# Kernel optimization log

Hardware: AMD Instinct MI355X
Metric: run time of the kernel (lower is better)

The kernel has to match this reference:

```python
import jax, jax.numpy as jnp
import numpy as np

IGNORE_INDEX = -100
BT, H, V = 2048, 4096, 32000


def setup_inputs() -> dict:
    key = jax.random.key(0)
    k1, k2, k3, k4 = jax.random.split(key, 4)
    _input = jax.random.normal(k1, (BT, H), dtype=jnp.float32) * 0.02
    lin_weight = jax.random.normal(k2, (V, H), dtype=jnp.float32) * 0.02
    bias = jnp.zeros((V,), dtype=jnp.float32)
    target = jax.random.randint(k3, (BT,), 0, V)
    loss_weights = jax.random.uniform(k4, (BT,), dtype=jnp.float32)
    reduce_sum_loss_weights = jnp.sum(loss_weights)  # scalar float32
    return {
        "lin_weight": lin_weight,
        "_input": _input,
        "target": target,
        "bias": bias,
        "loss_weights": loss_weights,
        "reduce_sum_loss_weights": reduce_sum_loss_weights,
        "grad_accumulation_steps": 1,
    }


def reference(lin_weight, _input, target, bias, loss_weights,
              reduce_sum_loss_weights, grad_accumulation_steps):
    # logits: (BT, V) -- the torch module chunks over BT to avoid materializing
    # this; as a correctness reference we compute it directly.
    logits = _input @ lin_weight.T + bias
    mask = target != IGNORE_INDEX                      # (BT,)
    n_non_ignore = jnp.maximum(mask.sum(), 1).astype(logits.dtype)
    safe_t = jnp.where(mask, target, 0)
    lse = jax.nn.logsumexp(logits, axis=-1)            # (BT,)
    gold = jnp.take_along_axis(logits, safe_t[:, None], axis=-1)[:, 0]
    # liger kernel with reduction='mean' divides per-row loss by n_non_ignore
    loss_1d = jnp.where(mask, (lse - gold) / n_non_ignore, 0.0)
    total = jnp.sum(loss_1d * loss_weights)
    rs = jnp.asarray(reduce_sum_loss_weights).reshape(())
    denom = jnp.where(rs == 0, 1.0, rs)
    loss = jnp.where(rs == 0, 0.0, total / denom)
    return loss / grad_accumulation_steps
```

## Files before the change

### kernel.cpp

```cpp
#include <hip/hip_runtime.h>
#include <hip/hip_bf16.h>
#include <math.h>

#define IGNORE_INDEX (-100)

constexpr int BT = 2048, H = 4096, V = 32000;
constexpr int BM = 256, BN = 256, BK = 64;
constexpr int KT = H / BK;
constexpr int MT2 = BT / BM;
constexpr int NT2 = V / BN;
constexpr int NCHUNK = NT2 * 4;

typedef int   i32x4  __attribute__((ext_vector_type(4)));
typedef int   i32x8  __attribute__((ext_vector_type(8)));
typedef float f32x16 __attribute__((ext_vector_type(16)));

#define SC8 120

__device__ __forceinline__ void gload_lds16(const char* g, char* l) {
  __builtin_amdgcn_global_load_lds(
      (const __attribute__((address_space(1))) unsigned int*)(g),
      (__attribute__((address_space(3))) unsigned int*)(l), 16, 0, 0);
}

#define BAR()        asm volatile("s_barrier" ::: "memory")
#define WAIT_VM(N)   asm volatile("s_waitcnt vmcnt(" #N ")" ::: "memory")
#define SB0()        __builtin_amdgcn_sched_barrier(0)

__global__ __launch_bounds__(256)
void convert_fp8(const float* __restrict__ src, char* __restrict__ dst,
                 int n8) {
  int i = blockIdx.x * blockDim.x + threadIdx.x;
  const int stride = gridDim.x * blockDim.x;
  for (; i < n8; i += stride) {
    const float4 f0 = ((const float4*)src)[2 * i];
    const float4 f1 = ((const float4*)src)[2 * i + 1];
    const float S = 128.f;
    int lo = 0, hi = 0;
    lo = __builtin_amdgcn_cvt_pk_fp8_f32(f0.x * S, f0.y * S, lo, false);
    lo = __builtin_amdgcn_cvt_pk_fp8_f32(f0.z * S, f0.w * S, lo, true);
    hi = __builtin_amdgcn_cvt_pk_fp8_f32(f1.x * S, f1.y * S, hi, false);
    hi = __builtin_amdgcn_cvt_pk_fp8_f32(f1.z * S, f1.w * S, hi, true);
    int2 v; v.x = lo; v.y = hi;
    ((int2*)dst)[i] = v;
  }
}

__global__ __launch_bounds__(512, 2)
void gemm_lse_3buf(const char* __restrict__ Wq,
                   const char* __restrict__ Xq,
                   const int* __restrict__ target,
                   const float* __restrict__ bias,
                   float* __restrict__ pM, float* __restrict__ pS,
                   float* __restrict__ gold)
{
  __shared__ char As[49152];
  __shared__ char Bs[49152];

  const int tid  = threadIdx.x;
  const int lane = tid & 63;
  const int wid  = tid >> 6;
  const int wr   = wid >> 2;
  const int wcol = wid & 3;

  const int bid = (int)blockIdx.x;
  const int swz = (bid & 7) * 125 + (bid >> 3);
  const int mt = swz & (MT2 - 1);
  const int nt = swz >> 3;
  const int m0 = mt * BM, n0 = nt * BN;

  const int l31 = lane & 31;
  const int h   = lane >> 5;
  const int r2  = (l31 >> 1) & 3;
  const int s0  = ((2 * h) ^ r2) << 4;
  const int s1  = ((2 * h + 1) ^ r2) << 4;
  const int abase = (wr * 128 + l31) * 64;
  const int bbase = (wcol * 64 + l31) * 64;

  const int srow  = lane >> 2;
  const int sslot = ((lane & 3) ^ ((lane >> 3) & 3)) << 4;

  const char* asrc = Xq + (size_t)(m0 + wid * 32 + srow) * H + sslot;
  const char* bsrc = Wq + (size_t)(n0 + wid * 32 + srow) * H + sslot;

  f32x16 acc[4][2] = {};
  i32x8 aF0, aF1, bF0, bF1;

#define STAGE_A(BUF, DT)                                                      \
  { gload_lds16(asrc + (DT) * BK,                                             \
                &As[(BUF) * 16384 + wid * 2048 + lane * 16]);                 \
    gload_lds16(asrc + (size_t)16 * H + (DT) * BK,                            \
                &As[(BUF) * 16384 + wid * 2048 + 1024 + lane * 16]); }

#define STAGE_B(BUF, DT)                                                      \
  { gload_lds16(bsrc + (DT) * BK,                                             \
                &Bs[(BUF) * 16384 + wid * 2048 + lane * 16]);                 \
    gload_lds16(bsrc + (size_t)16 * H + (DT) * BK,                            \
                &Bs[(BUF) * 16384 + wid * 2048 + 1024 + lane * 16]); }

#define RDA(DST, BUF, MI)                                                     \
  { i32x4 lo = *(const i32x4*)&As[(BUF) * 16384 + abase + (MI) * 2048 + s0];  \
    i32x4 hi = *(const i32x4*)&As[(BUF) * 16384 + abase + (MI) * 2048 + s1];  \
    DST[0] = lo[0]; DST[1] = lo[1]; DST[2] = lo[2]; DST[3] = lo[3];           \
    DST[4] = hi[0]; DST[5] = hi[1]; DST[6] = hi[2]; DST[7] = hi[3]; }

#define RDB(DST, BUF, NJ)                                                     \
  { i32x4 lo = *(const i32x4*)&Bs[(BUF) * 16384 + bbase + (NJ) * 2048 + s0];  \
    i32x4 hi = *(const i32x4*)&Bs[(BUF) * 16384 + bbase + (NJ) * 2048 + s1];  \
    DST[0] = lo[0]; DST[1] = lo[1]; DST[2] = lo[2]; DST[3] = lo[3];           \
    DST[4] = hi[0]; DST[5] = hi[1]; DST[6] = hi[2]; DST[7] = hi[3]; }

#define MFMA4(MH)                                                             \
  { __builtin_amdgcn_s_setprio(1);                                            \
    acc[(MH)*2+0][0] = __builtin_amdgcn_mfma_scale_f32_32x32x64_f8f6f4(       \
        aF0, bF0, acc[(MH)*2+0][0], 0, 0, 0, SC8, 0, SC8);                    \
    acc[(MH)*2+0][1] = __builtin_amdgcn_mfma_scale_f32_32x32x64_f8f6f4(       \
        aF0, bF1, acc[(MH)*2+0][1], 0, 0, 0, SC8, 0, SC8);                    \
    acc[(MH)*2+1][0] = __builtin_amdgcn_mfma_scale_f32_32x32x64_f8f6f4(       \
        aF1, bF0, acc[(MH)*2+1][0], 0, 0, 0, SC8, 0, SC8);                    \
    acc[(MH)*2+1][1] = __builtin_amdgcn_mfma_scale_f32_32x32x64_f8f6f4(       \
        aF1, bF1, acc[(MH)*2+1][1], 0, 0, 0, SC8, 0, SC8);                    \
    __builtin_amdgcn_s_setprio(0); }

#define PHASE(D, DOSTAGE, VMN)                                                \
  { if (DOSTAGE) { STAGE_B(((D) + 2) % 3, (D) + 2);                           \
                   STAGE_A(((D) + 2) % 3, (D) + 2); }                         \
    WAIT_VM(VMN);                                                             \
    RDA(aF0, (D) % 3, 0); RDA(aF1, (D) % 3, 1);                               \
    RDB(bF0, (D) % 3, 0); RDB(bF1, (D) % 3, 1);                               \
    MFMA4(0);                                                                 \
    RDA(aF0, (D) % 3, 2); RDA(aF1, (D) % 3, 3);                               \
    MFMA4(1);                                                                 \
    SB0(); BAR(); }

  STAGE_B(0, 0); STAGE_A(0, 0);
  STAGE_B(1, 1); STAGE_A(1, 1);
  WAIT_VM(4);
  BAR();

  for (int it = 0; it < 20; ++it) {
    PHASE(0, 1, 4);
    PHASE(1, 1, 4);
    PHASE(2, 1, 4);
    asrc += 3 * BK; bsrc += 3 * BK;
  }
  PHASE(0, 1, 4);
  PHASE(1, 1, 0);
  PHASE(2, 0, 0);
  RDA(aF0, 0, 0); RDA(aF1, 0, 1); RDB(bF0, 0, 0); RDB(bF1, 0, 1);
  MFMA4(0);
  RDA(aF0, 0, 2); RDA(aF1, 0, 3);
  MFMA4(1);

#undef PHASE
#undef STAGE_A
#undef STAGE_B
#undef RDA
#undef RDB
#undef MFMA4

  const int colbase = n0 + wcol * 64;
  float bv[2];
#pragma unroll
  for (int nj = 0; nj < 2; ++nj) bv[nj] = bias[colbase + nj * 32 + l31];

  const int chunk = nt * 4 + wcol;
#pragma unroll
  for (int mi = 0; mi < 4; ++mi) {
#pragma unroll
    for (int r = 0; r < 16; ++r) {
      const int row = m0 + wr * 128 + mi * 32 + (r & 3) + 8 * (r >> 2) + 4 * h;
      const float v0 = acc[mi][0][r] + bv[0];
      const float v1 = acc[mi][1][r] + bv[1];
      float mx = fmaxf(v0, v1);
#pragma unroll
      for (int d = 1; d < 32; d <<= 1) mx = fmaxf(mx, __shfl_xor(mx, d));
      float s = expf(v0 - mx) + expf(v1 - mx);
#pragma unroll
      for (int d = 1; d < 32; d <<= 1) s += __shfl_xor(s, d);
      if (l31 == 0) {
        pM[(size_t)row * NCHUNK + chunk] = mx;
        pS[(size_t)row * NCHUNK + chunk] = s;
      }
      const int t = target[row];
      const int d0 = t - colbase;
      if (d0 >= 0 && d0 < 64 && l31 == (d0 & 31)) {
        gold[row] = (d0 >> 5) ? v1 : v0;
      }
    }
  }
}

__global__ __launch_bounds__(256)
void reduce_lse(const float* __restrict__ pM, const float* __restrict__ pS,
                const float* __restrict__ gold, const int* __restrict__ target,
                const float* __restrict__ lw, float* __restrict__ rowterm)
{
  const int wid = threadIdx.x >> 6, lane = threadIdx.x & 63;
  const int row = blockIdx.x * 4 + wid;
  if (row >= BT) return;
  const float* pm = pM + (size_t)row * NCHUNK;
  const float* ps = pS + (size_t)row * NCHUNK;
  float m = -INFINITY;
  for (int c2 = lane; c2 < NCHUNK; c2 += 64) m = fmaxf(m, pm[c2]);
#pragma unroll
  for (int d = 1; d < 64; d <<= 1) m = fmaxf(m, __shfl_xor(m, d));
  float s = 0.f;
  for (int c2 = lane; c2 < NCHUNK; c2 += 64) s += ps[c2] * expf(pm[c2] - m);
#pragma unroll
  for (int d = 1; d < 64; d <<= 1) s += __shfl_xor(s, d);
  if (lane == 0) {
    const int t = target[row];
    float term = 0.f;
    if (t != IGNORE_INDEX) term = (m + logf(s) - gold[row]) * lw[row];
    rowterm[row] = term;
  }
}

__global__ __launch_bounds__(256)
void finalize(const float* __restrict__ rowterm, const int* __restrict__ target,
              const float* __restrict__ rsw, const int* __restrict__ gas,
              float* __restrict__ out)
{
  __shared__ float sred[4];
  __shared__ int cred[4];
  const int tid = threadIdx.x;
  float s = 0.f;
  int cnt = 0;
  for (int i = tid; i < BT; i += 256) {
    s += rowterm[i];
    cnt += (target[i] != IGNORE_INDEX) ? 1 : 0;
  }
#pragma unroll
  for (int d = 1; d < 64; d <<= 1) {
    s += __shfl_xor(s, d);
    cnt += __shfl_xor(cnt, d);
  }
  const int wid = tid >> 6, lane = tid & 63;
  if (lane == 0) { sred[wid] = s; cred[wid] = cnt; }
  __syncthreads();
  if (tid == 0) {
    const float st = sred[0] + sred[1] + sred[2] + sred[3];
    const int ct = cred[0] + cred[1] + cred[2] + cred[3];
    const float n = (float)((ct > 0) ? ct : 1);
    const float rs = rsw[0];
    float loss = (rs == 0.f) ? 0.f : (st / n) / rs;
    loss /= (float)gas[0];
    out[0] = loss;
  }
}

extern "C" void kernel_launch(void* const* d_in, const int* in_sizes, int n_in,
                              void* d_out, int out_size, void* d_ws, size_t ws_size,
                              hipStream_t stream)
{
  const float* Wt     = (const float*)d_in[0];
  const float* X      = (const float*)d_in[1];
  const int*   target = (const int*)d_in[2];
  const float* bias   = (const float*)d_in[3];
  const float* lw     = (const float*)d_in[4];
  const float* rsw    = (const float*)d_in[5];
  const int*   gas    = (const int*)d_in[6];
  float* out = (float*)d_out;

  const size_t nW = (size_t)V * H, nX = (size_t)BT * H;

  char* Wq = (char*)d_ws;
  char* Xq = Wq + nW;
  float* pM = (float*)(Xq + nX);
  float* pS = pM + (size_t)BT * NCHUNK;
  float* gold = pS + (size_t)BT * NCHUNK;
  float* rowterm = gold + BT;

  convert_fp8<<<dim3(2048), dim3(256), 0, stream>>>(Wt, Wq, (int)(nW / 8));
  convert_fp8<<<dim3(256), dim3(256), 0, stream>>>(X, Xq, (int)(nX / 8));
  gemm_lse_3buf<<<dim3(MT2 * NT2), dim3(512), 0, stream>>>(Wq, Xq, target,
                                                           bias, pM, pS, gold);
  reduce_lse<<<dim3(BT / 4), dim3(256), 0, stream>>>(pM, pS, gold, target, lw,
                                                     rowterm);
  finalize<<<dim3(1), dim3(256), 0, stream>>>(rowterm, target, rsw, gas, out);
}
```

Measured before the change: 600.5 us.

## Shrink GEMM tiles to 128x128 with 4 waves and move barrier before reads

Replaces the 256x256, 8-wave block tile with a 128x128, 4-wave tile and three blocks per CU, quadrupling the grid and halving accumulator state per wave. The barrier now sits after the load wait and before the LDS reads instead of at the end of each phase. The aim is better occupancy and tail balance across CUs. In exchange each block reuses less data from LDS, so global and L2 traffic rises, and with only one barrier per phase there is a possible race on buffer reuse.

```diff
diff --git a/kernel.cpp b/kernel.cpp
--- a/kernel.cpp
+++ b/kernel.cpp
@@ -5,11 +5,11 @@
 #define IGNORE_INDEX (-100)
 
 constexpr int BT = 2048, H = 4096, V = 32000;
-constexpr int BM = 256, BN = 256, BK = 64;
+constexpr int BM = 128, BN = 128, BK = 64;
 constexpr int KT = H / BK;
-constexpr int MT2 = BT / BM;
-constexpr int NT2 = V / BN;
-constexpr int NCHUNK = NT2 * 4;
+constexpr int MT = BT / BM;
+constexpr int NT = V / BN;
+constexpr int NCHUNK = NT * 2;
 
 typedef int   i32x4  __attribute__((ext_vector_type(4)));
 typedef int   i32x8  __attribute__((ext_vector_type(8)));
@@ -46,27 +46,27 @@
   }
 }
 
-__global__ __launch_bounds__(512, 2)
-void gemm_lse_3buf(const char* __restrict__ Wq,
-                   const char* __restrict__ Xq,
-                   const int* __restrict__ target,
-                   const float* __restrict__ bias,
-                   float* __restrict__ pM, float* __restrict__ pS,
-                   float* __restrict__ gold)
-{
-  __shared__ char As[49152];
-  __shared__ char Bs[49152];
+__global__ __launch_bounds__(256, 3)
+void gemm_lse_o3(const char* __restrict__ Wq,
+                 const char* __restrict__ Xq,
+                 const int* __restrict__ target,
+                 const float* __restrict__ bias,
+                 float* __restrict__ pM, float* __restrict__ pS,
+                 float* __restrict__ gold)
+{
+  __shared__ char As[24576];
+  __shared__ char Bs[24576];
 
   const int tid  = threadIdx.x;
   const int lane = tid & 63;
   const int wid  = tid >> 6;
-  const int wr   = wid >> 2;
-  const int wcol = wid & 3;
+  const int wr   = wid >> 1;
+  const int wc   = wid & 1;
 
   const int bid = (int)blockIdx.x;
-  const int swz = (bid & 7) * 125 + (bid >> 3);
-  const int mt = swz & (MT2 - 1);
-  const int nt = swz >> 3;
+  const int swz = (bid & 7) * 500 + (bid >> 3);
+  const int mt = swz & (MT - 1);
+  const int nt = swz >> 4;
   const int m0 = mt * BM, n0 = nt * BN;
 
   const int l31 = lane & 31;
@@ -74,8 +74,8 @@
   const int r2  = (l31 >> 1) & 3;
   const int s0  = ((2 * h) ^ r2) << 4;
   const int s1  = ((2 * h + 1) ^ r2) << 4;
-  const int abase = (wr * 128 + l31) * 64;
-  const int bbase = (wcol * 64 + l31) * 64;
+  const int abase = (wr * 64 + l31) * 64;
+  const int bbase = (wc * 64 + l31) * 64;
 
   const int srow  = lane >> 2;
   const int sslot = ((lane & 3) ^ ((lane >> 3) & 3)) << 4;
@@ -83,60 +83,57 @@
   const char* asrc = Xq + (size_t)(m0 + wid * 32 + srow) * H + sslot;
   const char* bsrc = Wq + (size_t)(n0 + wid * 32 + srow) * H + sslot;
 
-  f32x16 acc[4][2] = {};
+  f32x16 acc[2][2] = {};
   i32x8 aF0, aF1, bF0, bF1;
 
 #define STAGE_A(BUF, DT)                                                      \
   { gload_lds16(asrc + (DT) * BK,                                             \
-                &As[(BUF) * 16384 + wid * 2048 + lane * 16]);                 \
+                &As[(BUF) * 8192 + wid * 2048 + lane * 16]);                  \
     gload_lds16(asrc + (size_t)16 * H + (DT) * BK,                            \
-                &As[(BUF) * 16384 + wid * 2048 + 1024 + lane * 16]); }
+                &As[(BUF) * 8192 + wid * 2048 + 1024 + lane * 16]); }
 
 #define STAGE_B(BUF, DT)                                                      \
   { gload_lds16(bsrc + (DT) * BK,                                             \
-                &Bs[(BUF) * 16384 + wid * 2048 + lane * 16]);                 \
+                &Bs[(BUF) * 8192 + wid * 2048 + lane * 16]);                  \
     gload_lds16(bsrc + (size_t)16 * H + (DT) * BK,                            \
-                &Bs[(BUF) * 16384 + wid * 2048 + 1024 + lane * 16]); }
+                &Bs[(BUF) * 8192 + wid * 2048 + 1024 + lane * 16]); }
 
 #define RDA(DST, BUF, MI)                                                     \
-  { i32x4 lo = *(const i32x4*)&As[(BUF) * 16384 + abase + (MI) * 2048 + s0];  \
-    i32x4 hi = *(const i32x4*)&As[(BUF) * 16384 + abase + (MI) * 2048 + s1];  \
+  { i32x4 lo = *(const i32x4*)&As[(BUF) * 8192 + abase + (MI) * 2048 + s0];   \
+    i32x4 hi = *(const i32x4*)&As[(BUF) * 8192 + abase + (MI) * 2048 + s1];   \
     DST[0] = lo[0]; DST[1] = lo[1]; DST[2] = lo[2]; DST[3] = lo[3];           \
     DST[4] = hi[0]; DST[5] = hi[1]; DST[6] = hi[2]; DST[7] = hi[3]; }
 
 #define RDB(DST, BUF, NJ)                                                     \
-  { i32x4 lo = *(const i32x4*)&Bs[(BUF) * 16384 + bbase + (NJ) * 2048 + s0];  \
-    i32x4 hi = *(const i32x4*)&Bs[(BUF) * 16384 + bbase + (NJ) * 2048 + s1];  \
+  { i32x4 lo = *(const i32x4*)&Bs[(BUF) * 8192 + bbase + (NJ) * 2048 + s0];   \
+    i32x4 hi = *(const i32x4*)&Bs[(BUF) * 8192 + bbase + (NJ) * 2048 + s1];   \
     DST[0] = lo[0]; DST[1] = lo[1]; DST[2] = lo[2]; DST[3] = lo[3];           \
     DST[4] = hi[0]; DST[5] = hi[1]; DST[6] = hi[2]; DST[7] = hi[3]; }
 
-#define MFMA4(MH)                                                             \
+#define MFMA4()                                                               \
   { __builtin_amdgcn_s_setprio(1);                                            \
-    acc[(MH)*2+0][0] = __builtin_amdgcn_mfma_scale_f32_32x32x64_f8f6f4(       \
-        aF0, bF0, acc[(MH)*2+0][0], 0, 0, 0, SC8, 0, SC8);                    \
-    acc[(MH)*2+0][1] = __builtin_amdgcn_mfma_scale_f32_32x32x64_f8f6f4(       \
-        aF0, bF1, acc[(MH)*2+0][1], 0, 0, 0, SC8, 0, SC8);                    \
-    acc[(MH)*2+1][0] = __builtin_amdgcn_mfma_scale_f32_32x32x64_f8f6f4(       \
-        aF1, bF0, acc[(MH)*2+1][0], 0, 0, 0, SC8, 0, SC8);                    \
-    acc[(MH)*2+1][1] = __builtin_amdgcn_mfma_scale_f32_32x32x64_f8f6f4(       \
-        aF1, bF1, acc[(MH)*2+1][1], 0, 0, 0, SC8, 0, SC8);                    \
+    acc[0][0] = __builtin_amdgcn_mfma_scale_f32_32x32x64_f8f6f4(              \
+        aF0, bF0, acc[0][0], 0, 0, 0, SC8, 0, SC8);                           \
+    acc[0][1] = __builtin_amdgcn_mfma_scale_f32_32x32x64_f8f6f4(              \
+        aF0, bF1, acc[0][1], 0, 0, 0, SC8, 0, SC8);                           \
+    acc[1][0] = __builtin_amdgcn_mfma_scale_f32_32x32x64_f8f6f4(              \
+        aF1, bF0, acc[1][0], 0, 0, 0, SC8, 0, SC8);                           \
+    acc[1][1] = __builtin_amdgcn_mfma_scale_f32_32x32x64_f8f6f4(              \
+        aF1, bF1, acc[1][1], 0, 0, 0, SC8, 0, SC8);                           \
     __builtin_amdgcn_s_setprio(0); }
 
 #define PHASE(D, DOSTAGE, VMN)                                                \
   { if (DOSTAGE) { STAGE_B(((D) + 2) % 3, (D) + 2);                           \
                    STAGE_A(((D) + 2) % 3, (D) + 2); }                         \
     WAIT_VM(VMN);                                                             \
+    BAR();                                                                    \
     RDA(aF0, (D) % 3, 0); RDA(aF1, (D) % 3, 1);                               \
     RDB(bF0, (D) % 3, 0); RDB(bF1, (D) % 3, 1);                               \
-    MFMA4(0);                                                                 \
-    RDA(aF0, (D) % 3, 2); RDA(aF1, (D) % 3, 3);                               \
-    MFMA4(1);                                                                 \
-    SB0(); BAR(); }
+    MFMA4();                                                                  \
+    SB0(); }
 
   STAGE_B(0, 0); STAGE_A(0, 0);
   STAGE_B(1, 1); STAGE_A(1, 1);
-  WAIT_VM(4);
-  BAR();
 
   for (int it = 0; it < 20; ++it) {
     PHASE(0, 1, 4);
@@ -147,10 +144,9 @@
   PHASE(0, 1, 4);
   PHASE(1, 1, 0);
   PHASE(2, 0, 0);
+  BAR();
   RDA(aF0, 0, 0); RDA(aF1, 0, 1); RDB(bF0, 0, 0); RDB(bF1, 0, 1);
-  MFMA4(0);
-  RDA(aF0, 0, 2); RDA(aF1, 0, 3);
-  MFMA4(1);
+  MFMA4();
 
 #undef PHASE
 #undef STAGE_A
@@ -159,17 +155,17 @@
 #undef RDB
 #undef MFMA4
 
-  const int colbase = n0 + wcol * 64;
+  const int colbase = n0 + wc * 64;
   float bv[2];
 #pragma unroll
   for (int nj = 0; nj < 2; ++nj) bv[nj] = bias[colbase + nj * 32 + l31];
 
-  const int chunk = nt * 4 + wcol;
-#pragma unroll
-  for (int mi = 0; mi < 4; ++mi) {
+  const int chunk = nt * 2 + wc;
+#pragma unroll
+  for (int mi = 0; mi < 2; ++mi) {
 #pragma unroll
     for (int r = 0; r < 16; ++r) {
-      const int row = m0 + wr * 128 + mi * 32 + (r & 3) + 8 * (r >> 2) + 4 * h;
+      const int row = m0 + wr * 64 + mi * 32 + (r & 3) + 8 * (r >> 2) + 4 * h;
       const float v0 = acc[mi][0][r] + bv[0];
       const float v1 = acc[mi][1][r] + bv[1];
       float mx = fmaxf(v0, v1);
@@ -274,8 +270,8 @@
 
   convert_fp8<<<dim3(2048), dim3(256), 0, stream>>>(Wt, Wq, (int)(nW / 8));
   convert_fp8<<<dim3(256), dim3(256), 0, stream>>>(X, Xq, (int)(nX / 8));
-  gemm_lse_3buf<<<dim3(MT2 * NT2), dim3(512), 0, stream>>>(Wq, Xq, target,
-                                                           bias, pM, pS, gold);
+  gemm_lse_o3<<<dim3(MT * NT), dim3(256), 0, stream>>>(Wq, Xq, target,
+                                                       bias, pM, pS, gold);
   reduce_lse<<<dim3(BT / 4), dim3(256), 0, stream>>>(pM, pS, gold, target, lw,
                                                      rowterm);
   finalize<<<dim3(1), dim3(256), 0, stream>>>(rowterm, target, rsw, gas, out);
```

Measured after the change: 590.2 us. About the same (-1.7%).
